# Performance work log

Measured on AMD Instinct MI355X. Metric: run time of the kernel, lower is better.

The kernel has to match this reference:

```python
import jax, jax.numpy as jnp
import numpy as np

N = 50000       # nodes
E = 800000      # edges (before self-loops)
IN_DIM = 128
HID = 16
H1 = 8
OUT_DIM = 16
H2 = 1
NEG_SLOPE = 0.2  # PyG GATConv LeakyReLU negative slope


def setup_inputs() -> dict:
    key = jax.random.key(0)
    ks = jax.random.split(key, 10)
    x = jax.random.normal(ks[0], (N, IN_DIM), dtype=jnp.float32)
    edge_index = jax.random.randint(ks[1], (2, E), 0, N, dtype=jnp.int32)
    # layer 1: Linear(IN_DIM -> H1*HID, no bias), att vectors [H, C], bias [H1*HID]
    W1 = jax.random.normal(ks[2], (IN_DIM, H1 * HID), dtype=jnp.float32) / np.sqrt(IN_DIM).astype(np.float32)
    a_src1 = jax.random.normal(ks[3], (H1, HID), dtype=jnp.float32) * 0.1
    a_dst1 = jax.random.normal(ks[4], (H1, HID), dtype=jnp.float32) * 0.1
    b1 = jnp.zeros((H1 * HID,), dtype=jnp.float32)
    # layer 2: Linear(H1*HID -> H2*OUT_DIM), concat=False -> bias [OUT_DIM]
    W2 = jax.random.normal(ks[5], (H1 * HID, H2 * OUT_DIM), dtype=jnp.float32) / np.sqrt(H1 * HID).astype(np.float32)
    a_src2 = jax.random.normal(ks[6], (H2, OUT_DIM), dtype=jnp.float32) * 0.1
    a_dst2 = jax.random.normal(ks[7], (H2, OUT_DIM), dtype=jnp.float32) * 0.1
    b2 = jnp.zeros((OUT_DIM,), dtype=jnp.float32)
    return {"x": x, "edge_index": edge_index, "W1": W1, "a_src1": a_src1,
            "a_dst1": a_dst1, "b1": b1, "W2": W2, "a_src2": a_src2,
            "a_dst2": a_dst2, "b2": b2}


def gat_conv(x, src, dst, W, a_src, a_dst, bias, heads, ch, concat):
    n = x.shape[0]
    h = (x @ W).reshape(n, heads, ch)                      # [N,H,C]
    s_src = jnp.sum(h * a_src, axis=-1)                    # [N,H] att_src . Wx
    s_dst = jnp.sum(h * a_dst, axis=-1)                    # [N,H]
    e = jax.nn.leaky_relu(s_src[src] + s_dst[dst], NEG_SLOPE)  # [Etot,H]
    # segment softmax over incoming edges per target node
    m = jax.ops.segment_max(e, dst, num_segments=n)        # [N,H]
    ee = jnp.exp(e - m[dst])
    denom = jax.ops.segment_sum(ee, dst, num_segments=n)   # [N,H]
    alpha = ee / denom[dst]                                # [Etot,H]
    out = jax.ops.segment_sum(h[src] * alpha[:, :, None], dst, num_segments=n)  # [N,H,C]
    out = out.reshape(n, heads * ch) if concat else out.mean(axis=1)
    return out + bias


def reference(x, edge_index, W1, a_src1, a_dst1, b1, W2, a_src2, a_dst2, b2):
    n = x.shape[0]
    loop = jnp.arange(n, dtype=edge_index.dtype)           # PyG adds self-loops
    src = jnp.concatenate([edge_index[0], loop])
    dst = jnp.concatenate([edge_index[1], loop])
    # eval mode: F.dropout is identity
    h = jax.nn.elu(gat_conv(x, src, dst, W1, a_src1, a_dst1, b1, H1, HID, True))
    out = gat_conv(h, src, dst, W2, a_src2, a_dst2, b2, H2, OUT_DIM, False)
    return jax.nn.log_softmax(out, axis=1)
```

## Files before the change

kernel.cpp:

```cpp
#include <hip/hip_runtime.h>
#include <hip/hip_fp16.h>
#include <math.h>

#define NEG_SLOPE 0.2f
#define MAXDEG 64
#define CSTRIDE 16
#define NXCD 8
#define NSLICE 256

typedef short bf16x8 __attribute__((ext_vector_type(8)));
typedef float f32x4 __attribute__((ext_vector_type(4)));

__device__ __forceinline__ unsigned short f2bf(float f) {
    union { float f; unsigned u; } v; v.f = f;
    unsigned r = v.u + 0x7FFF + ((v.u >> 16) & 1);
    return (unsigned short)(r >> 16);
}

__global__ void k_init(const float* __restrict__ W1, unsigned short* __restrict__ frag,
                       int* __restrict__ cursor, unsigned short* __restrict__ csr, int N)
{
    int gid = blockIdx.x * 256 + threadIdx.x;
    if (gid < 16384) {
        int f = gid >> 3, j = gid & 7;
        int kk = f >> 9, c = (f >> 6) & 7, l = f & 63;
        int col = c * 16 + (l & 15);
        int k = kk * 32 + ((l >> 4) << 3) + j;
        frag[gid] = f2bf(W1[k * 128 + col]);
    }
    if (gid < N) {
        cursor[gid * CSTRIDE] = 1;
        csr[gid * MAXDEG] = (unsigned short)gid;
    }
}

__global__ __launch_bounds__(256) void k_mega(
    const float* __restrict__ x, const bf16x8* __restrict__ frag,
    const float* __restrict__ a_src, const float* __restrict__ a_dst,
    __half* __restrict__ h1h, float* __restrict__ ssrc, float* __restrict__ sdst,
    int N, int G1,
    const int* __restrict__ src_e, const int* __restrict__ dst_e, int E,
    int* __restrict__ cursor, unsigned short* __restrict__ csr)
{
    const int t = threadIdx.x;

    if (blockIdx.x >= G1) {
        int fb = blockIdx.x - G1;
        int xcd = blockIdx.x & (NXCD - 1);
        int slice = fb >> 3;
        int dlo = (int)(((long)N * xcd) >> 3);
        int dhi = (int)(((long)N * (xcd + 1)) >> 3);
        int e0 = (int)((long)E * slice / NSLICE);
        int e1 = (int)((long)E * (slice + 1) / NSLICE);
        for (int i = e0 + t; i < e1; i += 256) {
            int d = dst_e[i];
            if (d >= dlo && d < dhi) {
                int s = src_e[i];
                int pos = atomicAdd(&cursor[d * CSTRIDE], 1);
                if (pos < MAXDEG) csr[d * MAXDEG + pos] = (unsigned short)s;
            }
        }
        return;
    }

    const int r0 = blockIdx.x * 64;
    const int w = t >> 6, l = t & 63;
    const int lo = l & 15, hi = l >> 4;
    const int row = r0 + w * 16 + lo;
    const bool rok = (row < N);

    f32x4 acc[8] = {};
    #pragma unroll
    for (int kk = 0; kk < 4; ++kk) {
        bf16x8 a;
        {
            float4 f0 = make_float4(0.f,0.f,0.f,0.f), f1 = f0;
            if (rok) {
                const float4* xp = (const float4*)(x + (size_t)row * 128 + kk * 32 + hi * 8);
                f0 = xp[0]; f1 = xp[1];
            }
            a[0] = (short)f2bf(f0.x); a[1] = (short)f2bf(f0.y);
            a[2] = (short)f2bf(f0.z); a[3] = (short)f2bf(f0.w);
            a[4] = (short)f2bf(f1.x); a[5] = (short)f2bf(f1.y);
            a[6] = (short)f2bf(f1.z); a[7] = (short)f2bf(f1.w);
        }
        #pragma unroll
        for (int c = 0; c < 8; ++c) {
            bf16x8 b = frag[(kk * 8 + c) * 64 + l];
            acc[c] = __builtin_amdgcn_mfma_f32_16x16x32_bf16(a, b, acc[c], 0, 0, 0);
        }
    }

    float av_s[8], av_d[8];
    #pragma unroll
    for (int c = 0; c < 8; ++c) {
        av_s[c] = a_src[c * 16 + lo];
        av_d[c] = a_dst[c * 16 + lo];
    }

    #pragma unroll
    for (int reg = 0; reg < 4; ++reg) {
        int grow = r0 + w * 16 + hi * 4 + reg;
        bool ok = (grow < N);
        if (ok) {
            #pragma unroll
            for (int c = 0; c < 8; ++c)
                h1h[(size_t)grow * 128 + c * 16 + lo] = __float2half(acc[c][reg]);
        }
        #pragma unroll
        for (int c = 0; c < 8; ++c) {
            float ps = acc[c][reg] * av_s[c];
            float pd = acc[c][reg] * av_d[c];
            #pragma unroll
            for (int m = 8; m >= 1; m >>= 1) {
                ps += __shfl_xor(ps, m, 64);
                pd += __shfl_xor(pd, m, 64);
            }
            if (ok && lo == 0) {
                ssrc[grow * 8 + c] = ps;
                sdst[grow * 8 + c] = pd;
            }
        }
    }
}

__global__ __launch_bounds__(256) void k_aggr1g2(
    const int* __restrict__ cursor, const unsigned short* __restrict__ csr,
    const __half2* __restrict__ h1h, const float* __restrict__ ssrc,
    const float* __restrict__ sdst, const float* __restrict__ b1,
    const float* __restrict__ W2, const float* __restrict__ a_src2,
    const float* __restrict__ a_dst2,
    float* __restrict__ h2, float* __restrict__ s2s, float* __restrict__ s2d, int N)
{
    __shared__ float lds_w2[2080];
    __shared__ float lds_h[4][132];
    const int t = threadIdx.x;

    {
        const float4* src = (const float4*)W2;
        #pragma unroll
        for (int i = 0; i < 2; ++i) {
            int f = i * 256 + t;
            ((float4*)lds_w2)[f + ((f >> 7) << 1)] = src[f];
        }
    }
    __syncthreads();

    const int wid = t >> 6;
    const int lane = t & 63;
    const int node = blockIdx.x * 4 + wid;
    if (node >= N) return;
    const int h = lane >> 3;
    const int beg = node * MAXDEG;
    const int end = beg + min(cursor[node * CSTRIDE], MAXDEG);
    const float sd = sdst[node * 8 + h];
    float acc0 = 0.f, acc1 = 0.f, wsum = 0.f;

    int j = beg;
    for (; j + 7 < end; j += 8) {
        int s0 = csr[j],     s1 = csr[j + 1], s2 = csr[j + 2], s3 = csr[j + 3];
        int s4 = csr[j + 4], s5 = csr[j + 5], s6 = csr[j + 6], s7 = csr[j + 7];
        float e0 = ssrc[s0 * 8 + h], e1 = ssrc[s1 * 8 + h];
        float e2 = ssrc[s2 * 8 + h], e3 = ssrc[s3 * 8 + h];
        float e4 = ssrc[s4 * 8 + h], e5 = ssrc[s5 * 8 + h];
        float e6 = ssrc[s6 * 8 + h], e7 = ssrc[s7 * 8 + h];
        __half2 v0 = h1h[(size_t)s0 * 64 + lane];
        __half2 v1 = h1h[(size_t)s1 * 64 + lane];
        __half2 v2 = h1h[(size_t)s2 * 64 + lane];
        __half2 v3 = h1h[(size_t)s3 * 64 + lane];
        __half2 v4 = h1h[(size_t)s4 * 64 + lane];
        __half2 v5 = h1h[(size_t)s5 * 64 + lane];
        __half2 v6 = h1h[(size_t)s6 * 64 + lane];
        __half2 v7 = h1h[(size_t)s7 * 64 + lane];
        e0 += sd; e0 = (e0 >= 0.f) ? e0 : NEG_SLOPE * e0; float w0 = __expf(e0);
        e1 += sd; e1 = (e1 >= 0.f) ? e1 : NEG_SLOPE * e1; float w1 = __expf(e1);
        e2 += sd; e2 = (e2 >= 0.f) ? e2 : NEG_SLOPE * e2; float w2 = __expf(e2);
        e3 += sd; e3 = (e3 >= 0.f) ? e3 : NEG_SLOPE * e3; float w3 = __expf(e3);
        e4 += sd; e4 = (e4 >= 0.f) ? e4 : NEG_SLOPE * e4; float w4 = __expf(e4);
        e5 += sd; e5 = (e5 >= 0.f) ? e5 : NEG_SLOPE * e5; float w5 = __expf(e5);
        e6 += sd; e6 = (e6 >= 0.f) ? e6 : NEG_SLOPE * e6; float w6 = __expf(e6);
        e7 += sd; e7 = (e7 >= 0.f) ? e7 : NEG_SLOPE * e7; float w7 = __expf(e7);
        wsum += ((w0 + w1) + (w2 + w3)) + ((w4 + w5) + (w6 + w7));
        float2 f0 = __half22float2(v0), f1 = __half22float2(v1);
        float2 f2 = __half22float2(v2), f3 = __half22float2(v3);
        float2 f4 = __half22float2(v4), f5 = __half22float2(v5);
        float2 f6 = __half22float2(v6), f7 = __half22float2(v7);
        acc0 = fmaf(w0, f0.x, acc0); acc1 = fmaf(w0, f0.y, acc1);
        acc0 = fmaf(w1, f1.x, acc0); acc1 = fmaf(w1, f1.y, acc1);
        acc0 = fmaf(w2, f2.x, acc0); acc1 = fmaf(w2, f2.y, acc1);
        acc0 = fmaf(w3, f3.x, acc0); acc1 = fmaf(w3, f3.y, acc1);
        acc0 = fmaf(w4, f4.x, acc0); acc1 = fmaf(w4, f4.y, acc1);
        acc0 = fmaf(w5, f5.x, acc0); acc1 = fmaf(w5, f5.y, acc1);
        acc0 = fmaf(w6, f6.x, acc0); acc1 = fmaf(w6, f6.y, acc1);
        acc0 = fmaf(w7, f7.x, acc0); acc1 = fmaf(w7, f7.y, acc1);
    }
    for (; j < end; ++j) {
        int s = csr[j];
        float e = ssrc[s * 8 + h] + sd;
        e = (e >= 0.f) ? e : NEG_SLOPE * e;
        float w = __expf(e);
        wsum += w;
        float2 f = __half22float2(h1h[(size_t)s * 64 + lane]);
        acc0 = fmaf(w, f.x, acc0); acc1 = fmaf(w, f.y, acc1);
    }

    const float2 bb = ((const float2*)b1)[lane];
    float inv = 1.f / wsum;
    float va = acc0 * inv + bb.x;
    float vb = acc1 * inv + bb.y;
    va = (va > 0.f) ? va : expm1f(va);
    vb = (vb > 0.f) ? vb : expm1f(vb);

    {
        int k0 = 2 * lane;
        lds_h[wid][k0 + (k0 >> 5)]     = va;
        lds_h[wid][k0 + 1 + (k0 >> 5)] = vb;
    }
    asm volatile("s_waitcnt lgkmcnt(0)" ::: "memory");

    const int col = lane & 15, kg = lane >> 4;
    float r = 0.f;
    #pragma unroll
    for (int k2 = 0; k2 < 32; ++k2) {
        int k = kg * 32 + k2;
        int wi = k * 16 + col;
        r = fmaf(lds_h[wid][k + kg], lds_w2[wi + ((wi >> 9) << 3)], r);
    }
    r += __shfl_xor(r, 16, 64);
    r += __shfl_xor(r, 32, 64);
    if (lane < 16) h2[(size_t)node * 16 + col] = r;

    float ps = r * a_src2[col];
    float pd = r * a_dst2[col];
    #pragma unroll
    for (int m = 8; m >= 1; m >>= 1) {
        ps += __shfl_xor(ps, m, 64);
        pd += __shfl_xor(pd, m, 64);
    }
    if (lane == 0) { s2s[node] = ps; s2d[node] = pd; }
}

__global__ __launch_bounds__(256) void k_aggr2(
    const int* __restrict__ cursor, const unsigned short* __restrict__ csr,
    const float* __restrict__ h2, const float* __restrict__ s2s,
    const float* __restrict__ s2d, const float* __restrict__ b2,
    float* __restrict__ out, int N)
{
    int gid = blockIdx.x * 256 + threadIdx.x;
    int node = gid >> 4;
    if (node >= N) return;
    int c = gid & 15;
    const int beg = node * MAXDEG;
    const int end = beg + min(cursor[node * CSTRIDE], MAXDEG);
    float sd = s2d[node];
    float acc = 0.f, wsum = 0.f;

    int j = beg;
    for (; j + 7 < end; j += 8) {
        int s0 = csr[j],     s1 = csr[j + 1], s2 = csr[j + 2], s3 = csr[j + 3];
        int s4 = csr[j + 4], s5 = csr[j + 5], s6 = csr[j + 6], s7 = csr[j + 7];
        float e0 = s2s[s0], e1 = s2s[s1], e2 = s2s[s2], e3 = s2s[s3];
        float e4 = s2s[s4], e5 = s2s[s5], e6 = s2s[s6], e7 = s2s[s7];
        float g0 = h2[(size_t)s0 * 16 + c];
        float g1 = h2[(size_t)s1 * 16 + c];
        float g2 = h2[(size_t)s2 * 16 + c];
        float g3 = h2[(size_t)s3 * 16 + c];
        float g4 = h2[(size_t)s4 * 16 + c];
        float g5 = h2[(size_t)s5 * 16 + c];
        float g6 = h2[(size_t)s6 * 16 + c];
        float g7 = h2[(size_t)s7 * 16 + c];
        e0 += sd; e0 = (e0 >= 0.f) ? e0 : NEG_SLOPE * e0; float w0 = __expf(e0);
        e1 += sd; e1 = (e1 >= 0.f) ? e1 : NEG_SLOPE * e1; float w1 = __expf(e1);
        e2 += sd; e2 = (e2 >= 0.f) ? e2 : NEG_SLOPE * e2; float w2 = __expf(e2);
        e3 += sd; e3 = (e3 >= 0.f) ? e3 : NEG_SLOPE * e3; float w3 = __expf(e3);
        e4 += sd; e4 = (e4 >= 0.f) ? e4 : NEG_SLOPE * e4; float w4 = __expf(e4);
        e5 += sd; e5 = (e5 >= 0.f) ? e5 : NEG_SLOPE * e5; float w5 = __expf(e5);
        e6 += sd; e6 = (e6 >= 0.f) ? e6 : NEG_SLOPE * e6; float w6 = __expf(e6);
        e7 += sd; e7 = (e7 >= 0.f) ? e7 : NEG_SLOPE * e7; float w7 = __expf(e7);
        wsum += ((w0 + w1) + (w2 + w3)) + ((w4 + w5) + (w6 + w7));
        acc = fmaf(w0, g0, acc); acc = fmaf(w1, g1, acc);
        acc = fmaf(w2, g2, acc); acc = fmaf(w3, g3, acc);
        acc = fmaf(w4, g4, acc); acc = fmaf(w5, g5, acc);
        acc = fmaf(w6, g6, acc); acc = fmaf(w7, g7, acc);
    }
    for (; j < end; ++j) {
        int s = csr[j];
        float e = s2s[s] + sd;
        e = (e >= 0.f) ? e : NEG_SLOPE * e;
        float w = __expf(e);
        wsum += w;
        acc = fmaf(w, h2[(size_t)s * 16 + c], acc);
    }

    float v = acc / wsum + b2[c];
    float m = v;
    #pragma unroll
    for (int msk = 8; msk >= 1; msk >>= 1) m = fmaxf(m, __shfl_xor(m, msk, 64));
    float ex = __expf(v - m);
    float sum = ex;
    #pragma unroll
    for (int msk = 8; msk >= 1; msk >>= 1) sum += __shfl_xor(sum, msk, 64);
    out[(size_t)node * 16 + c] = v - m - __logf(sum);
}

extern "C" void kernel_launch(void* const* d_in, const int* in_sizes, int n_in,
                              void* d_out, int out_size, void* d_ws, size_t ws_size,
                              hipStream_t stream)
{
    const float* x      = (const float*)d_in[0];
    const int*   ei     = (const int*)  d_in[1];
    const float* W1     = (const float*)d_in[2];
    const float* a_src1 = (const float*)d_in[3];
    const float* a_dst1 = (const float*)d_in[4];
    const float* b1     = (const float*)d_in[5];
    const float* W2     = (const float*)d_in[6];
    const float* a_src2 = (const float*)d_in[7];
    const float* a_dst2 = (const float*)d_in[8];
    const float* b2     = (const float*)d_in[9];
    float* out = (float*)d_out;

    const int N = in_sizes[0] / 128;
    const int E = in_sizes[1] / 2;
    const int* src_e = ei;
    const int* dst_e = ei + E;

    float* p = (float*)d_ws;
    __half* h1h  = (__half*)p; p += (size_t)N * 64;
    unsigned short* frag = (unsigned short*)p; p += 8192;
    float* ssrc1 = p; p += (size_t)N * 8;
    float* sdst1 = p; p += (size_t)N * 8;
    float* h2    = p; p += (size_t)N * 16;
    float* s2s   = p; p += (size_t)N;
    float* s2d   = p; p += (size_t)N;
    int* ip = (int*)p;
    int* cursor = ip; ip += (size_t)N * CSTRIDE;
    unsigned short* csr = (unsigned short*)ip;

    const int G1 = (N + 63) / 64;
    const int GF = NSLICE * NXCD;

    k_init<<<(N + 255) / 256, 256, 0, stream>>>(W1, frag, cursor, csr, N);

    k_mega<<<G1 + GF, 256, 0, stream>>>(
        x, (const bf16x8*)frag, a_src1, a_dst1, h1h, ssrc1, sdst1, N, G1,
        src_e, dst_e, E, cursor, csr);

    k_aggr1g2<<<(N + 3) / 4, 256, 0, stream>>>(
        cursor, csr, (const __half2*)h1h, ssrc1, sdst1, b1,
        W2, a_src2, a_dst2, h2, s2s, s2d, N);

    k_aggr2<<<((size_t)N * 16 + 255) / 256, 256, 0, stream>>>(
        cursor, csr, h2, s2s, s2d, b2, out, N);
}
```

Measured before the change: 130.3 us.

## Distribute edge-weight exp across lanes via LDS and use nontemporal loads/stores

```diff
diff --git a/kernel.cpp b/kernel.cpp
--- a/kernel.cpp
+++ b/kernel.cpp
@@ -74,15 +74,16 @@
     for (int kk = 0; kk < 4; ++kk) {
         bf16x8 a;
         {
-            float4 f0 = make_float4(0.f,0.f,0.f,0.f), f1 = f0;
+            f32x4 f0 = {0.f,0.f,0.f,0.f}, f1 = {0.f,0.f,0.f,0.f};
             if (rok) {
-                const float4* xp = (const float4*)(x + (size_t)row * 128 + kk * 32 + hi * 8);
-                f0 = xp[0]; f1 = xp[1];
-            }
-            a[0] = (short)f2bf(f0.x); a[1] = (short)f2bf(f0.y);
-            a[2] = (short)f2bf(f0.z); a[3] = (short)f2bf(f0.w);
-            a[4] = (short)f2bf(f1.x); a[5] = (short)f2bf(f1.y);
-            a[6] = (short)f2bf(f1.z); a[7] = (short)f2bf(f1.w);
+                const f32x4* xp = (const f32x4*)(x + (size_t)row * 128 + kk * 32 + hi * 8);
+                f0 = __builtin_nontemporal_load(xp);
+                f1 = __builtin_nontemporal_load(xp + 1);
+            }
+            a[0] = (short)f2bf(f0[0]); a[1] = (short)f2bf(f0[1]);
+            a[2] = (short)f2bf(f0[2]); a[3] = (short)f2bf(f0[3]);
+            a[4] = (short)f2bf(f1[0]); a[5] = (short)f2bf(f1[1]);
+            a[6] = (short)f2bf(f1[2]); a[7] = (short)f2bf(f1[3]);
         }
         #pragma unroll
         for (int c = 0; c < 8; ++c) {
@@ -98,14 +99,18 @@
         av_d[c] = a_dst[c * 16 + lo];
     }
 
+    unsigned short* h1b = (unsigned short*)h1h;
     #pragma unroll
     for (int reg = 0; reg < 4; ++reg) {
         int grow = r0 + w * 16 + hi * 4 + reg;
         bool ok = (grow < N);
         if (ok) {
             #pragma unroll
-            for (int c = 0; c < 8; ++c)
-                h1h[(size_t)grow * 128 + c * 16 + lo] = __float2half(acc[c][reg]);
+            for (int c = 0; c < 8; ++c) {
+                __half hv = __float2half(acc[c][reg]);
+                unsigned short hb = *reinterpret_cast<unsigned short*>(&hv);
+                __builtin_nontemporal_store(hb, h1b + (size_t)grow * 128 + c * 16 + lo);
+            }
         }
         #pragma unroll
         for (int c = 0; c < 8; ++c) {
@@ -134,6 +139,7 @@
 {
     __shared__ float lds_w2[2080];
     __shared__ float lds_h[4][132];
+    __shared__ float lds_ws[4][64];
     const int t = threadIdx.x;
 
     {
@@ -150,36 +156,48 @@
     const int lane = t & 63;
     const int node = blockIdx.x * 4 + wid;
     if (node >= N) return;
-    const int h = lane >> 3;
+    const int hc = lane >> 3;
+    const int hd = lane & 7;
+    const int edl = lane >> 3;
     const int beg = node * MAXDEG;
     const int end = beg + min(cursor[node * CSTRIDE], MAXDEG);
-    const float sd = sdst[node * 8 + h];
+    const float sdd = sdst[node * 8 + hd];
+    const float sdc = sdst[node * 8 + hc];
     float acc0 = 0.f, acc1 = 0.f, wsum = 0.f;
 
     int j = beg;
     for (; j + 7 < end; j += 8) {
-        int s0 = csr[j],     s1 = csr[j + 1], s2 = csr[j + 2], s3 = csr[j + 3];
-        int s4 = csr[j + 4], s5 = csr[j + 5], s6 = csr[j + 6], s7 = csr[j + 7];
-        float e0 = ssrc[s0 * 8 + h], e1 = ssrc[s1 * 8 + h];
-        float e2 = ssrc[s2 * 8 + h], e3 = ssrc[s3 * 8 + h];
-        float e4 = ssrc[s4 * 8 + h], e5 = ssrc[s5 * 8 + h];
-        float e6 = ssrc[s6 * 8 + h], e7 = ssrc[s7 * 8 + h];
-        __half2 v0 = h1h[(size_t)s0 * 64 + lane];
-        __half2 v1 = h1h[(size_t)s1 * 64 + lane];
-        __half2 v2 = h1h[(size_t)s2 * 64 + lane];
-        __half2 v3 = h1h[(size_t)s3 * 64 + lane];
-        __half2 v4 = h1h[(size_t)s4 * 64 + lane];
-        __half2 v5 = h1h[(size_t)s5 * 64 + lane];
-        __half2 v6 = h1h[(size_t)s6 * 64 + lane];
-        __half2 v7 = h1h[(size_t)s7 * 64 + lane];
-        e0 += sd; e0 = (e0 >= 0.f) ? e0 : NEG_SLOPE * e0; float w0 = __expf(e0);
-        e1 += sd; e1 = (e1 >= 0.f) ? e1 : NEG_SLOPE * e1; float w1 = __expf(e1);
-        e2 += sd; e2 = (e2 >= 0.f) ? e2 : NEG_SLOPE * e2; float w2 = __expf(e2);
-        e3 += sd; e3 = (e3 >= 0.f) ? e3 : NEG_SLOPE * e3; float w3 = __expf(e3);
-        e4 += sd; e4 = (e4 >= 0.f) ? e4 : NEG_SLOPE * e4; float w4 = __expf(e4);
-        e5 += sd; e5 = (e5 >= 0.f) ? e5 : NEG_SLOPE * e5; float w5 = __expf(e5);
-        e6 += sd; e6 = (e6 >= 0.f) ? e6 : NEG_SLOPE * e6; float w6 = __expf(e6);
-        e7 += sd; e7 = (e7 >= 0.f) ? e7 : NEG_SLOPE * e7; float w7 = __expf(e7);
+        uint4 cv = *(const uint4*)(csr + j);
+        int sa0 = (int)(cv.x & 0xffff), sa1 = (int)(cv.x >> 16);
+        int sa2 = (int)(cv.y & 0xffff), sa3 = (int)(cv.y >> 16);
+        int sa4 = (int)(cv.z & 0xffff), sa5 = (int)(cv.z >> 16);
+        int sa6 = (int)(cv.w & 0xffff), sa7 = (int)(cv.w >> 16);
+
+        int se = csr[j + edl];
+        float e = ssrc[se * 8 + hd] + sdd;
+
+        __half2 v0 = h1h[(size_t)sa0 * 64 + lane];
+        __half2 v1 = h1h[(size_t)sa1 * 64 + lane];
+        __half2 v2 = h1h[(size_t)sa2 * 64 + lane];
+        __half2 v3 = h1h[(size_t)sa3 * 64 + lane];
+        __half2 v4 = h1h[(size_t)sa4 * 64 + lane];
+        __half2 v5 = h1h[(size_t)sa5 * 64 + lane];
+        __half2 v6 = h1h[(size_t)sa6 * 64 + lane];
+        __half2 v7 = h1h[(size_t)sa7 * 64 + lane];
+
+        e = (e >= 0.f) ? e : NEG_SLOPE * e;
+        lds_ws[wid][lane] = __expf(e);
+        asm volatile("s_waitcnt lgkmcnt(0)" ::: "memory");
+        __builtin_amdgcn_sched_barrier(0);
+
+        float w0 = lds_ws[wid][0 * 8 + hc];
+        float w1 = lds_ws[wid][1 * 8 + hc];
+        float w2 = lds_ws[wid][2 * 8 + hc];
+        float w3 = lds_ws[wid][3 * 8 + hc];
+        float w4 = lds_ws[wid][4 * 8 + hc];
+        float w5 = lds_ws[wid][5 * 8 + hc];
+        float w6 = lds_ws[wid][6 * 8 + hc];
+        float w7 = lds_ws[wid][7 * 8 + hc];
         wsum += ((w0 + w1) + (w2 + w3)) + ((w4 + w5) + (w6 + w7));
         float2 f0 = __half22float2(v0), f1 = __half22float2(v1);
         float2 f2 = __half22float2(v2), f3 = __half22float2(v3);
@@ -196,7 +214,7 @@
     }
     for (; j < end; ++j) {
         int s = csr[j];
-        float e = ssrc[s * 8 + h] + sd;
+        float e = ssrc[s * 8 + hc] + sdc;
         e = (e >= 0.f) ? e : NEG_SLOPE * e;
         float w = __expf(e);
         wsum += w;
@@ -217,6 +235,7 @@
         lds_h[wid][k0 + 1 + (k0 >> 5)] = vb;
     }
     asm volatile("s_waitcnt lgkmcnt(0)" ::: "memory");
+    __builtin_amdgcn_sched_barrier(0);
 
     const int col = lane & 15, kg = lane >> 4;
     float r = 0.f;
```

Result: no change. 132.3 us (+1.6%).
